# Kernel tuning notes

Hardware: AMD Instinct MI355X
Metric: run time of the kernel (lower is better)

## Reference

```python
import jax, jax.numpy as jnp
import numpy as np

TOKENS, D_IN, FEATURES = 8192, 4096, 16384


def setup_inputs() -> dict:
    key = jax.random.key(0)
    k1, k2, k3, k4 = jax.random.split(key, 4)
    inputs = jax.random.normal(k1, (TOKENS, D_IN), dtype=jnp.float32)
    # int4-valued kernel stored as int32 (values in [0, 8) stand in for int4 codes)
    kernel = jax.random.randint(k2, (D_IN, FEATURES), 0, 8, dtype=jnp.int32)
    # per-output-channel scale; keep strictly positive to avoid div-by-zero
    scale = jax.random.uniform(k3, (1, FEATURES), dtype=jnp.float32) + 0.5
    bias = jax.random.normal(k4, (FEATURES,), dtype=jnp.float32)
    return {"inputs": inputs, "kernel": kernel, "scale": scale, "bias": bias}


def reference(inputs, kernel, scale, bias):
    # Dequantize int4 kernel: upcast + per-channel scale division, then GEMM.
    w = kernel.astype(inputs.dtype) / scale          # [D_IN, FEATURES]
    y = inputs @ w                                   # [TOKENS, FEATURES]
    return y + bias
```

## Files before the change

### kernel.cpp

```cpp
#include <hip/hip_runtime.h>

#define TOKENS 8192
#define D_IN   4096
#define FEATS  16384
#define NT     (D_IN / 128)
#define NIT    (NT / 2)

typedef __attribute__((ext_vector_type(4))) int   i4v;
typedef __attribute__((ext_vector_type(4))) float f32x4;

__device__ __forceinline__ void gload_lds16(const void* g, void* l) {
  __builtin_amdgcn_global_load_lds(
      (const __attribute__((address_space(1))) void*)g,
      (__attribute__((address_space(3))) void*)l, 16, 0, 0);
}

__device__ __forceinline__ int pack4(float4 f, float inv) {
  int a = __float2int_rn(f.x * inv), b = __float2int_rn(f.y * inv),
      c = __float2int_rn(f.z * inv), d = __float2int_rn(f.w * inv);
  return (a & 0xff) | ((b & 0xff) << 8) | ((c & 0xff) << 16) | ((d & 0xff) << 24);
}

__global__ __launch_bounds__(256) void quant_x_kernel(const float* __restrict__ x,
                                                      signed char* __restrict__ xq,
                                                      float* __restrict__ xs) {
  const int row = blockIdx.x, t = threadIdx.x;
  const float* xr = x + (long)row * D_IN;
  float4 v0 = *(const float4*)(xr + t * 16 + 0);
  float4 v1 = *(const float4*)(xr + t * 16 + 4);
  float4 v2 = *(const float4*)(xr + t * 16 + 8);
  float4 v3 = *(const float4*)(xr + t * 16 + 12);
  float m = 0.f;
  m = fmaxf(m, fmaxf(fmaxf(fabsf(v0.x), fabsf(v0.y)), fmaxf(fabsf(v0.z), fabsf(v0.w))));
  m = fmaxf(m, fmaxf(fmaxf(fabsf(v1.x), fabsf(v1.y)), fmaxf(fabsf(v1.z), fabsf(v1.w))));
  m = fmaxf(m, fmaxf(fmaxf(fabsf(v2.x), fabsf(v2.y)), fmaxf(fabsf(v2.z), fabsf(v2.w))));
  m = fmaxf(m, fmaxf(fmaxf(fabsf(v3.x), fabsf(v3.y)), fmaxf(fabsf(v3.z), fabsf(v3.w))));
#pragma unroll
  for (int off = 32; off >= 1; off >>= 1) m = fmaxf(m, __shfl_xor(m, off));
  __shared__ float wm[4];
  if ((t & 63) == 0) wm[t >> 6] = m;
  __syncthreads();
  m = fmaxf(fmaxf(wm[0], wm[1]), fmaxf(wm[2], wm[3]));
  m = fmaxf(m, 1e-20f);
  const float inv = 127.f / m;
  if (t == 0) xs[row] = m / 127.f;
  int4 o;
  o.x = pack4(v0, inv); o.y = pack4(v1, inv);
  o.z = pack4(v2, inv); o.w = pack4(v3, inv);
  *(int4*)(xq + (long)row * D_IN + t * 16) = o;
}

__global__ __launch_bounds__(256) void wtrans8_kernel(const int* __restrict__ kq,
                                                      signed char* __restrict__ wt) {
  __shared__ signed char tile[64][68];
  const int n0 = blockIdx.x * 64, k0 = blockIdx.y * 64;
  const int t = threadIdx.x;
  const int kr = t >> 4, nc = (t & 15) * 4;
#pragma unroll
  for (int p = 0; p < 4; p++) {
    int4 v = *(const int4*)(kq + (long)(k0 + kr + 16 * p) * FEATS + n0 + nc);
    tile[kr + 16 * p][nc + 0] = (signed char)v.x;
    tile[kr + 16 * p][nc + 1] = (signed char)v.y;
    tile[kr + 16 * p][nc + 2] = (signed char)v.z;
    tile[kr + 16 * p][nc + 3] = (signed char)v.w;
  }
  __syncthreads();
  const int nr = t >> 4, kc = (t & 15) * 4;
#pragma unroll
  for (int p = 0; p < 4; p++) {
    int n = nr + 16 * p;
    int o = (tile[kc + 0][n] & 0xff) | ((tile[kc + 1][n] & 0xff) << 8) |
            ((tile[kc + 2][n] & 0xff) << 16) | ((tile[kc + 3][n] & 0xff) << 24);
    *(int*)(wt + (long)(n0 + n) * D_IN + k0 + kc) = o;
  }
}

#define BAR        __builtin_amdgcn_s_barrier()
#define VMCNT6     asm volatile("s_waitcnt vmcnt(6)" ::: "memory")
#define VMCNT0     asm volatile("s_waitcnt vmcnt(0)" ::: "memory")
#define PRIO1      __builtin_amdgcn_s_setprio(1)
#define PRIO0      __builtin_amdgcn_s_setprio(0)

#define TILEBASE(B_, MAT) (smem + (B_) * 65536 + (MAT) * 32768)

#define STAGE_A(B_, R0, KT) do { if ((KT) < NT) \
  gload_lds16(Xq + (m0 + (R0) + sr) * (long)D_IN + (long)(KT) * 128 + sgb, \
              TILEBASE(B_, 0) + (R0) * 128 + wid * 1024); } while (0)
#define STAGE_B(B_, R0, KT) do { if ((KT) < NT) \
  gload_lds16(Wq + (n0 + (R0) + sr) * (long)D_IN + (long)(KT) * 128 + sgb, \
              TILEBASE(B_, 1) + (R0) * 128 + wid * 1024); } while (0)

#define LDA1(B_, I) do { \
  const char* _p = TILEBASE(B_, 0) + (wr * 128 + (I) * 16 + rl) * 128; \
  aF[(I) & 3][0] = *(const i4v*)(_p + koff0); \
  aF[(I) & 3][1] = *(const i4v*)(_p + koff1); } while (0)
#define LDA4(B_, H) do { LDA1(B_, (H)*4+0); LDA1(B_, (H)*4+1); LDA1(B_, (H)*4+2); LDA1(B_, (H)*4+3); } while (0)
#define LDB1(B_, J) do { \
  const char* _p = TILEBASE(B_, 1) + (wc * 64 + (J) * 16 + rl) * 128; \
  bF[J][0] = *(const i4v*)(_p + koff0); \
  bF[J][1] = *(const i4v*)(_p + koff1); } while (0)
#define LDB4(B_) do { LDB1(B_, 0); LDB1(B_, 1); LDB1(B_, 2); LDB1(B_, 3); } while (0)

#define MM1(I, J, KS) \
  acc[I][J] = __builtin_amdgcn_mfma_i32_16x16x64_i8(aF[(I) & 3][KS], bF[J][KS], acc[I][J], 0, 0, 0)
#define MM16(H, JH) do { \
  MM1((H)*4+0,(JH)*2+0,0); MM1((H)*4+0,(JH)*2+0,1); \
  MM1((H)*4+0,(JH)*2+1,0); MM1((H)*4+0,(JH)*2+1,1); \
  MM1((H)*4+1,(JH)*2+0,0); MM1((H)*4+1,(JH)*2+0,1); \
  MM1((H)*4+1,(JH)*2+1,0); MM1((H)*4+1,(JH)*2+1,1); \
  MM1((H)*4+2,(JH)*2+0,0); MM1((H)*4+2,(JH)*2+0,1); \
  MM1((H)*4+2,(JH)*2+1,0); MM1((H)*4+2,(JH)*2+1,1); \
  MM1((H)*4+3,(JH)*2+0,0); MM1((H)*4+3,(JH)*2+0,1); \
  MM1((H)*4+3,(JH)*2+1,0); MM1((H)*4+3,(JH)*2+1,1); } while (0)

#define EP_PITCH 260
#define EP_HALF  (64 * EP_PITCH)

__global__ __launch_bounds__(512, 2) void gemm8i_kernel(
    const signed char* __restrict__ Xq,
    const signed char* __restrict__ Wq,
    const float* __restrict__ xs,
    const float* __restrict__ scale,
    const float* __restrict__ bias,
    float* __restrict__ C) {
  __shared__ __attribute__((aligned(16))) char smem[133120];

  const int tid = threadIdx.x;
  const int lane = tid & 63, wid = tid >> 6;
  const int wr = wid >> 2, wc = wid & 3;
  const int rl = lane & 15, q = lane >> 4;

  const int bid  = blockIdx.x;
  const int xcd  = bid & 7;
  const int l    = bid >> 3;
  const int rect = l >> 5;
  const int r    = l & 31;
  const int mloc = r & 3;
  const int nl   = r >> 2;
  const long m0 = (long)(xcd * 4 + mloc) * 256;
  const long n0 = (long)(rect * 8 + nl) * 256;

  const int sr = tid >> 3;
  const int sgb = ((tid & 7) ^ (sr & 7)) * 16;

  const int xm = (rl & 7) << 4;
  const int koff0 = (q * 16) ^ xm;
  const int koff1 = (64 + q * 16) ^ xm;

  i4v acc[8][4] = {};
  i4v aF[4][2], bF[4][2];

  STAGE_B(0, 0, 0); STAGE_B(0, 64, 0); STAGE_B(0, 128, 0); STAGE_B(0, 192, 0);
  STAGE_A(0, 0, 0); STAGE_A(0, 64, 0); STAGE_A(0, 128, 0); STAGE_A(0, 192, 0);
  STAGE_B(1, 0, 1); STAGE_B(1, 64, 1); STAGE_B(1, 128, 1); STAGE_B(1, 192, 1);
  STAGE_A(1, 0, 1); STAGE_A(1, 128, 1);
  VMCNT6;
  BAR;

  for (int it = 0; it < NIT; ++it) {
    const int t1 = 2 * it + 1, t2 = 2 * it + 2, t3 = 2 * it + 3;
    LDA4(0, 0); LDB4(0);
    STAGE_A(1, 64, t1); STAGE_A(1, 192, t1);
    PRIO1; MM16(0, 0); PRIO0; BAR;
    STAGE_A(0, 0, t2); STAGE_A(0, 128, t2);
    PRIO1; MM16(0, 1); PRIO0; BAR;
    LDA4(0, 1);
    STAGE_B(0, 0, t2); STAGE_B(0, 64, t2);
    PRIO1; MM16(1, 0); PRIO0; BAR;
    STAGE_B(0, 128, t2); STAGE_B(0, 192, t2);
    PRIO1; MM16(1, 1); PRIO0;
    if (it == NIT - 1) { VMCNT0; } else { VMCNT6; }
    BAR;
    LDA4(1, 0); LDB4(1);
    STAGE_A(0, 64, t2); STAGE_A(0, 192, t2);
    PRIO1; MM16(0, 0); PRIO0; BAR;
    STAGE_A(1, 0, t3); STAGE_A(1, 128, t3);
    PRIO1; MM16(0, 1); PRIO0; BAR;
    LDA4(1, 1);
    STAGE_B(1, 0, t3); STAGE_B(1, 64, t3);
    PRIO1; MM16(1, 0); PRIO0; BAR;
    STAGE_B(1, 128, t3); STAGE_B(1, 192, t3);
    PRIO1; MM16(1, 1); PRIO0;
    VMCNT6;
    BAR;
  }

  float rsv[4], bvv[4];
#pragma unroll
  for (int j = 0; j < 4; j++) {
    const long col = n0 + wc * 64 + j * 16 + rl;
    rsv[j] = 1.0f / scale[col];
    bvv[j] = bias[col];
  }
  float* ldsF = (float*)smem;
#pragma unroll
  for (int p = 0; p < 2; ++p) {
    if (p) BAR;
#pragma unroll
    for (int i = 0; i < 4; ++i) {
      const int ii = p * 4 + i;
      const long grow0 = m0 + wr * 128 + ii * 16 + q * 4;
#pragma unroll
      for (int r2 = 0; r2 < 4; ++r2) {
        const float xv = xs[grow0 + r2];
        const int lrow = i * 16 + q * 4 + r2;
        float* dst = ldsF + wr * EP_HALF + lrow * EP_PITCH;
#pragma unroll
        for (int j = 0; j < 4; ++j)
          dst[wc * 64 + j * 16 + rl] = (float)acc[ii][j][r2] * xv * rsv[j] + bvv[j];
      }
    }
    BAR;
#pragma unroll
    for (int h = 0; h < 2; ++h) {
      const int rr = wid * 8 + (lane >> 3);
      const long grow = m0 + h * 128 + p * 64 + rr;
      const float* src = ldsF + h * EP_HALF + rr * EP_PITCH + (lane & 7) * 4;
      float* crow = C + grow * (long)FEATS + n0 + (lane & 7) * 4;
#pragma unroll
      for (int g = 0; g < 8; ++g) {
        f32x4 v = *(const f32x4*)(src + g * 32);
        *(f32x4*)(crow + g * 32) = v;
      }
    }
  }
}

__global__ void naive_kernel(const float* __restrict__ x, const int* __restrict__ kq,
                             const float* __restrict__ scale, const float* __restrict__ bias,
                             float* __restrict__ out) {
  __shared__ float xa[16][16];
  __shared__ float wb[16][17];
  const int n = blockIdx.x * 16 + threadIdx.x;
  const int m = blockIdx.y * 16 + threadIdx.y;
  float accv = 0.f;
  for (int k0 = 0; k0 < D_IN; k0 += 16) {
    xa[threadIdx.y][threadIdx.x] = x[(long)m * D_IN + k0 + threadIdx.x];
    wb[threadIdx.y][threadIdx.x] = (float)kq[(long)(k0 + threadIdx.y) * FEATS + n];
    __syncthreads();
#pragma unroll
    for (int kk = 0; kk < 16; kk++) accv += xa[threadIdx.y][kk] * wb[kk][threadIdx.x];
    __syncthreads();
  }
  out[(long)m * FEATS + n] = accv * (1.0f / scale[n]) + bias[n];
}

extern "C" void kernel_launch(void* const* d_in, const int* in_sizes, int n_in,
                              void* d_out, int out_size, void* d_ws, size_t ws_size,
                              hipStream_t stream) {
  const float* x     = (const float*)d_in[0];
  const int*   kq    = (const int*)d_in[1];
  const float* scale = (const float*)d_in[2];
  const float* bias  = (const float*)d_in[3];
  float* out = (float*)d_out;

  const size_t need = (size_t)TOKENS * D_IN + (size_t)FEATS * D_IN + TOKENS * 4;
  if (ws_size < need) {
    naive_kernel<<<dim3(FEATS / 16, TOKENS / 16), dim3(16, 16), 0, stream>>>(
        x, kq, scale, bias, out);
    return;
  }

  signed char* Xq = (signed char*)d_ws;
  signed char* Wq = Xq + (size_t)TOKENS * D_IN;
  float* xs = (float*)(Wq + (size_t)FEATS * D_IN);

  quant_x_kernel<<<TOKENS, 256, 0, stream>>>(x, Xq, xs);
  wtrans8_kernel<<<dim3(FEATS / 64, D_IN / 64), dim3(256), 0, stream>>>(kq, Wq);
  gemm8i_kernel<<<dim3((TOKENS / 256) * (FEATS / 256)), 512, 0, stream>>>(
      Xq, Wq, xs, scale, bias, out);
}
```

Measured before the change: 612.4 us.

## Simplify GEMM main loop to plain double-buffered prefetch with full drain

Replaces the finely interleaved staging schedule, which used partial vmcnt waits and four barriers per K-tile, with a simpler double-buffer scheme. Each K-tile now issues all next-tile global-to-LDS loads at once, runs the MFMAs, then waits for every outstanding load and hits a single barrier. This cuts barrier count and scheduling complexity. The cost is less overlap of loads with compute, because memory must fully drain before each tile ends.

```diff
diff --git a/kernel.cpp b/kernel.cpp
--- a/kernel.cpp
+++ b/kernel.cpp
@@ -76,7 +76,6 @@
 }
 
 #define BAR        __builtin_amdgcn_s_barrier()
-#define VMCNT6     asm volatile("s_waitcnt vmcnt(6)" ::: "memory")
 #define VMCNT0     asm volatile("s_waitcnt vmcnt(0)" ::: "memory")
 #define PRIO1      __builtin_amdgcn_s_setprio(1)
 #define PRIO0      __builtin_amdgcn_s_setprio(0)
@@ -89,6 +88,9 @@
 #define STAGE_B(B_, R0, KT) do { if ((KT) < NT) \
   gload_lds16(Wq + (n0 + (R0) + sr) * (long)D_IN + (long)(KT) * 128 + sgb, \
               TILEBASE(B_, 1) + (R0) * 128 + wid * 1024); } while (0)
+#define STAGE_ALL(B_, KT) do { \
+  STAGE_A(B_, 0, KT); STAGE_A(B_, 64, KT); STAGE_A(B_, 128, KT); STAGE_A(B_, 192, KT); \
+  STAGE_B(B_, 0, KT); STAGE_B(B_, 64, KT); STAGE_B(B_, 128, KT); STAGE_B(B_, 192, KT); } while (0)
 
 #define LDA1(B_, I) do { \
   const char* _p = TILEBASE(B_, 0) + (wr * 128 + (I) * 16 + rl) * 128; \
@@ -113,6 +115,14 @@
   MM1((H)*4+3,(JH)*2+0,0); MM1((H)*4+3,(JH)*2+0,1); \
   MM1((H)*4+3,(JH)*2+1,0); MM1((H)*4+3,(JH)*2+1,1); } while (0)
 
+#define KTILE(B_, TN) do { \
+  LDA4(B_, 0); LDB4(B_); \
+  STAGE_ALL(B_ ^ 1, TN); \
+  PRIO1; MM16(0, 0); MM16(0, 1); PRIO0; \
+  LDA4(B_, 1); \
+  PRIO1; MM16(1, 0); MM16(1, 1); PRIO0; \
+  VMCNT0; BAR; } while (0)
+
 #define EP_PITCH 260
 #define EP_HALF  (64 * EP_PITCH)
 
@@ -150,39 +160,13 @@
   i4v acc[8][4] = {};
   i4v aF[4][2], bF[4][2];
 
-  STAGE_B(0, 0, 0); STAGE_B(0, 64, 0); STAGE_B(0, 128, 0); STAGE_B(0, 192, 0);
-  STAGE_A(0, 0, 0); STAGE_A(0, 64, 0); STAGE_A(0, 128, 0); STAGE_A(0, 192, 0);
-  STAGE_B(1, 0, 1); STAGE_B(1, 64, 1); STAGE_B(1, 128, 1); STAGE_B(1, 192, 1);
-  STAGE_A(1, 0, 1); STAGE_A(1, 128, 1);
-  VMCNT6;
+  STAGE_ALL(0, 0);
+  VMCNT0;
   BAR;
 
   for (int it = 0; it < NIT; ++it) {
-    const int t1 = 2 * it + 1, t2 = 2 * it + 2, t3 = 2 * it + 3;
-    LDA4(0, 0); LDB4(0);
-    STAGE_A(1, 64, t1); STAGE_A(1, 192, t1);
-    PRIO1; MM16(0, 0); PRIO0; BAR;
-    STAGE_A(0, 0, t2); STAGE_A(0, 128, t2);
-    PRIO1; MM16(0, 1); PRIO0; BAR;
-    LDA4(0, 1);
-    STAGE_B(0, 0, t2); STAGE_B(0, 64, t2);
-    PRIO1; MM16(1, 0); PRIO0; BAR;
-    STAGE_B(0, 128, t2); STAGE_B(0, 192, t2);
-    PRIO1; MM16(1, 1); PRIO0;
-    if (it == NIT - 1) { VMCNT0; } else { VMCNT6; }
-    BAR;
-    LDA4(1, 0); LDB4(1);
-    STAGE_A(0, 64, t2); STAGE_A(0, 192, t2);
-    PRIO1; MM16(0, 0); PRIO0; BAR;
-    STAGE_A(1, 0, t3); STAGE_A(1, 128, t3);
-    PRIO1; MM16(0, 1); PRIO0; BAR;
-    LDA4(1, 1);
-    STAGE_B(1, 0, t3); STAGE_B(1, 64, t3);
-    PRIO1; MM16(1, 0); PRIO0; BAR;
-    STAGE_B(1, 128, t3); STAGE_B(1, 192, t3);
-    PRIO1; MM16(1, 1); PRIO0;
-    VMCNT6;
-    BAR;
+    KTILE(0, 2 * it + 1);
+    KTILE(1, 2 * it + 2);
   }
 
   float rsv[4], bvv[4];
```

Measured after the change: 633.8 us. 1.04x slower.

## Switch int8 GEMM to 32x32x32 MFMA tiles and move scaling to store

Applied to the files above, without the earlier changes.

Replaces the 16x16x64 int8 MFMA fragments with 32x32x32 int8 MFMAs, reshaping the A/B register fragments, LDS read offsets and accumulator layout (16-wide vectors). The larger instruction covers more output per LDS fragment read, so each wave issues fewer LDS reads and fewer MFMA instructions. The epilogue is reorganised too: the column scale is applied when writing to LDS, while the row scale and a vectorised bias load are applied at the coalesced global store. The cost is heavier register pressure and a new swizzle mapping, which could cause bank conflicts or spills.

```diff
diff --git a/kernel.cpp b/kernel.cpp
--- a/kernel.cpp
+++ b/kernel.cpp
@@ -6,8 +6,9 @@
 #define NT     (D_IN / 128)
 #define NIT    (NT / 2)
 
-typedef __attribute__((ext_vector_type(4))) int   i4v;
-typedef __attribute__((ext_vector_type(4))) float f32x4;
+typedef __attribute__((ext_vector_type(4)))  int   i4v;
+typedef __attribute__((ext_vector_type(16))) int   i16v;
+typedef __attribute__((ext_vector_type(4)))  float f32x4;
 
 __device__ __forceinline__ void gload_lds16(const void* g, void* l) {
   __builtin_amdgcn_global_load_lds(
@@ -90,28 +91,22 @@
   gload_lds16(Wq + (n0 + (R0) + sr) * (long)D_IN + (long)(KT) * 128 + sgb, \
               TILEBASE(B_, 1) + (R0) * 128 + wid * 1024); } while (0)
 
-#define LDA1(B_, I) do { \
-  const char* _p = TILEBASE(B_, 0) + (wr * 128 + (I) * 16 + rl) * 128; \
-  aF[(I) & 3][0] = *(const i4v*)(_p + koff0); \
-  aF[(I) & 3][1] = *(const i4v*)(_p + koff1); } while (0)
-#define LDA4(B_, H) do { LDA1(B_, (H)*4+0); LDA1(B_, (H)*4+1); LDA1(B_, (H)*4+2); LDA1(B_, (H)*4+3); } while (0)
-#define LDB1(B_, J) do { \
-  const char* _p = TILEBASE(B_, 1) + (wc * 64 + (J) * 16 + rl) * 128; \
-  bF[J][0] = *(const i4v*)(_p + koff0); \
-  bF[J][1] = *(const i4v*)(_p + koff1); } while (0)
-#define LDB4(B_) do { LDB1(B_, 0); LDB1(B_, 1); LDB1(B_, 2); LDB1(B_, 3); } while (0)
-
-#define MM1(I, J, KS) \
-  acc[I][J] = __builtin_amdgcn_mfma_i32_16x16x64_i8(aF[(I) & 3][KS], bF[J][KS], acc[I][J], 0, 0, 0)
-#define MM16(H, JH) do { \
-  MM1((H)*4+0,(JH)*2+0,0); MM1((H)*4+0,(JH)*2+0,1); \
-  MM1((H)*4+0,(JH)*2+1,0); MM1((H)*4+0,(JH)*2+1,1); \
-  MM1((H)*4+1,(JH)*2+0,0); MM1((H)*4+1,(JH)*2+0,1); \
-  MM1((H)*4+1,(JH)*2+1,0); MM1((H)*4+1,(JH)*2+1,1); \
-  MM1((H)*4+2,(JH)*2+0,0); MM1((H)*4+2,(JH)*2+0,1); \
-  MM1((H)*4+2,(JH)*2+1,0); MM1((H)*4+2,(JH)*2+1,1); \
-  MM1((H)*4+3,(JH)*2+0,0); MM1((H)*4+3,(JH)*2+0,1); \
-  MM1((H)*4+3,(JH)*2+1,0); MM1((H)*4+3,(JH)*2+1,1); } while (0)
+#define LDA_H(B_, H) do { \
+  _Pragma("unroll") for (int _m = 0; _m < 2; ++_m) \
+  _Pragma("unroll") for (int _k = 0; _k < 4; ++_k) \
+    aF[_m][_k] = *(const i4v*)(TILEBASE(B_, 0) + \
+        (wr * 128 + (H) * 64 + _m * 32 + rl5) * 128 + kof[_k]); } while (0)
+#define LDB_ALL(B_) do { \
+  _Pragma("unroll") for (int _n = 0; _n < 2; ++_n) \
+  _Pragma("unroll") for (int _k = 0; _k < 4; ++_k) \
+    bF[_n][_k] = *(const i4v*)(TILEBASE(B_, 1) + \
+        (wc * 64 + _n * 32 + rl5) * 128 + kof[_k]); } while (0)
+
+#define MM8(H, J) do { \
+  _Pragma("unroll") for (int _k = 0; _k < 4; ++_k) { \
+    acc[(H)*2+0][J] = __builtin_amdgcn_mfma_i32_32x32x32_i8(aF[0][_k], bF[J][_k], acc[(H)*2+0][J], 0, 0, 0); \
+    acc[(H)*2+1][J] = __builtin_amdgcn_mfma_i32_32x32x32_i8(aF[1][_k], bF[J][_k], acc[(H)*2+1][J], 0, 0, 0); \
+  } } while (0)
 
 #define EP_PITCH 260
 #define EP_HALF  (64 * EP_PITCH)
@@ -128,7 +123,7 @@
   const int tid = threadIdx.x;
   const int lane = tid & 63, wid = tid >> 6;
   const int wr = wid >> 2, wc = wid & 3;
-  const int rl = lane & 15, q = lane >> 4;
+  const int rl5 = lane & 31, hi = lane >> 5;
 
   const int bid  = blockIdx.x;
   const int xcd  = bid & 7;
@@ -143,12 +138,13 @@
   const int sr = tid >> 3;
   const int sgb = ((tid & 7) ^ (sr & 7)) * 16;
 
-  const int xm = (rl & 7) << 4;
-  const int koff0 = (q * 16) ^ xm;
-  const int koff1 = (64 + q * 16) ^ xm;
-
-  i4v acc[8][4] = {};
-  i4v aF[4][2], bF[4][2];
+  const int xm = (lane & 7) << 4;
+  int kof[4];
+#pragma unroll
+  for (int _k = 0; _k < 4; ++_k) kof[_k] = ((_k << 5) | (hi << 4)) ^ xm;
+
+  i16v acc[4][2] = {};
+  i4v aF[2][4], bF[2][4];
 
   STAGE_B(0, 0, 0); STAGE_B(0, 64, 0); STAGE_B(0, 128, 0); STAGE_B(0, 192, 0);
   STAGE_A(0, 0, 0); STAGE_A(0, 64, 0); STAGE_A(0, 128, 0); STAGE_A(0, 192, 0);
@@ -159,68 +155,68 @@
 
   for (int it = 0; it < NIT; ++it) {
     const int t1 = 2 * it + 1, t2 = 2 * it + 2, t3 = 2 * it + 3;
-    LDA4(0, 0); LDB4(0);
+    LDA_H(0, 0); LDB_ALL(0);
     STAGE_A(1, 64, t1); STAGE_A(1, 192, t1);
-    PRIO1; MM16(0, 0); PRIO0; BAR;
+    PRIO1; MM8(0, 0); PRIO0; BAR;
     STAGE_A(0, 0, t2); STAGE_A(0, 128, t2);
-    PRIO1; MM16(0, 1); PRIO0; BAR;
-    LDA4(0, 1);
+    PRIO1; MM8(0, 1); PRIO0; BAR;
+    LDA_H(0, 1);
     STAGE_B(0, 0, t2); STAGE_B(0, 64, t2);
-    PRIO1; MM16(1, 0); PRIO0; BAR;
+    PRIO1; MM8(1, 0); PRIO0; BAR;
     STAGE_B(0, 128, t2); STAGE_B(0, 192, t2);
-    PRIO1; MM16(1, 1); PRIO0;
+    PRIO1; MM8(1, 1); PRIO0;
     if (it == NIT - 1) { VMCNT0; } else { VMCNT6; }
     BAR;
-    LDA4(1, 0); LDB4(1);
+    LDA_H(1, 0); LDB_ALL(1);
     STAGE_A(0, 64, t2); STAGE_A(0, 192, t2);
-    PRIO1; MM16(0, 0); PRIO0; BAR;
+    PRIO1; MM8(0, 0); PRIO0; BAR;
     STAGE_A(1, 0, t3); STAGE_A(1, 128, t3);
-    PRIO1; MM16(0, 1); PRIO0; BAR;
-    LDA4(1, 1);
+    PRIO1; MM8(0, 1); PRIO0; BAR;
+    LDA_H(1, 1);
     STAGE_B(1, 0, t3); STAGE_B(1, 64, t3);
-    PRIO1; MM16(1, 0); PRIO0; BAR;
+    PRIO1; MM8(1, 0); PRIO0; BAR;
     STAGE_B(1, 128, t3); STAGE_B(1, 192, t3);
-    PRIO1; MM16(1, 1); PRIO0;
+    PRIO1; MM8(1, 1); PRIO0;
     VMCNT6;
     BAR;
   }
 
-  float rsv[4], bvv[4];
-#pragma unroll
-  for (int j = 0; j < 4; j++) {
-    const long col = n0 + wc * 64 + j * 16 + rl;
-    rsv[j] = 1.0f / scale[col];
-    bvv[j] = bias[col];
-  }
+  float rsv[2];
+#pragma unroll
+  for (int nJ = 0; nJ < 2; ++nJ)
+    rsv[nJ] = 1.0f / scale[n0 + wc * 64 + nJ * 32 + rl5];
+  f32x4 bias4[8];
+#pragma unroll
+  for (int g = 0; g < 8; ++g)
+    bias4[g] = *(const f32x4*)(bias + n0 + g * 32 + (lane & 7) * 4);
+
   float* ldsF = (float*)smem;
 #pragma unroll
   for (int p = 0; p < 2; ++p) {
     if (p) BAR;
 #pragma unroll
-    for (int i = 0; i < 4; ++i) {
-      const int ii = p * 4 + i;
-      const long grow0 = m0 + wr * 128 + ii * 16 + q * 4;
-#pragma unroll
-      for (int r2 = 0; r2 < 4; ++r2) {
-        const float xv = xs[grow0 + r2];
-        const int lrow = i * 16 + q * 4 + r2;
-        float* dst = ldsF + wr * EP_HALF + lrow * EP_PITCH;
-#pragma unroll
-        for (int j = 0; j < 4; ++j)
-          dst[wc * 64 + j * 16 + rl] = (float)acc[ii][j][r2] * xv * rsv[j] + bvv[j];
+    for (int mIh = 0; mIh < 2; ++mIh) {
+      const int mI = p * 2 + mIh;
+#pragma unroll
+      for (int rg = 0; rg < 16; ++rg) {
+        const int lrow = mIh * 32 + (rg & 3) + 8 * (rg >> 2) + 4 * hi;
+        float* dst = ldsF + wr * EP_HALF + lrow * EP_PITCH + wc * 64 + rl5;
+        dst[0]  = (float)acc[mI][0][rg] * rsv[0];
+        dst[32] = (float)acc[mI][1][rg] * rsv[1];
       }
     }
     BAR;
+    const int rr = wid * 8 + (lane >> 3);
 #pragma unroll
     for (int h = 0; h < 2; ++h) {
-      const int rr = wid * 8 + (lane >> 3);
       const long grow = m0 + h * 128 + p * 64 + rr;
+      const float xsr = xs[grow];
       const float* src = ldsF + h * EP_HALF + rr * EP_PITCH + (lane & 7) * 4;
       float* crow = C + grow * (long)FEATS + n0 + (lane & 7) * 4;
 #pragma unroll
       for (int g = 0; g < 8; ++g) {
         f32x4 v = *(const f32x4*)(src + g * 32);
-        *(f32x4*)(crow + g * 32) = v;
+        *(f32x4*)(crow + g * 32) = v * xsr + bias4[g];
       }
     }
   }
```

Result: slower. 664.0 us (+8.4%).
